# Kernel optimization log

Measured on AMD Instinct MI355X. Metric: run time of the kernel, lower is better.

## Reference

```python
import jax, jax.numpy as jnp
import numpy as np

N_NODES = 100000
N_EDGES = 1600000
HIDDEN = 64
LEAKY_SLOPE = 0.01  # torch F.leaky_relu default


def setup_inputs() -> dict:
    key = jax.random.key(0)
    k1, k2, k3, k4 = jax.random.split(key, 4)
    x = jax.random.normal(k1, (N_NODES, HIDDEN), dtype=jnp.float32)
    edge_index = jax.random.randint(k2, (2, N_EDGES), 0, N_NODES, dtype=jnp.int64)
    # Linear(hidden, 1, bias=False) weights, squeezed to [hidden]
    w_i = jax.random.normal(k3, (HIDDEN,), dtype=jnp.float32) * 0.1
    w_j = jax.random.normal(k4, (HIDDEN,), dtype=jnp.float32) * 0.1
    return {"x": x, "edge_index": edge_index, "w_i": w_i, "w_j": w_j}


def reference(x, edge_index, w_i, w_j):
    n = x.shape[0]
    ej, ei = edge_index[0], edge_index[1]  # (edge_index_j, edge_index_i)
    # per-node attention scores, then per-edge gather
    s_i = x @ w_i  # [N]
    s_j = x @ w_j  # [N]
    e = jax.nn.leaky_relu(s_i[ei] + s_j[ej], LEAKY_SLOPE)  # [E]
    # segment softmax over edges grouped by destination node ei
    emax = jax.ops.segment_max(e, ei, num_segments=n)  # [N]
    ex = jnp.exp(e - emax[ei])  # [E]
    denom = jax.ops.segment_sum(ex, ei, num_segments=n)  # [N]
    alpha = ex / denom[ei]  # [E]
    # spmm: out[i] = sum_{edges e: dst=i} alpha_e * x[src_e]
    out = jax.ops.segment_sum(alpha[:, None] * x[ej], ei, num_segments=n)  # [N, H]
    return jax.nn.relu(out)
```

## Files before the change

### kernel.cpp

```cpp
#include <hip/hip_runtime.h>
#include <stdint.h>

#define N_NODES 100000
#define N_EDGES 1600000
#define HIDDEN  64
#define SLOPE   0.01f
#define NBUCK   782
#define CAPB    2816
#define PCHUNK  16384
#define NPART   98
#define NSB     391
#define NCAP    48
#define NSTRIDE 50


__device__ __forceinline__ unsigned short f2bf(float f) {
    uint32_t u = __float_as_uint(f);
    uint32_t r = u + 0x7FFFu + ((u >> 16) & 1u);
    return (unsigned short)(r >> 16);
}

__global__ void __launch_bounds__(1024) k_build(const float* __restrict__ x,
                                                const float* __restrict__ w_i,
                                                const float* __restrict__ w_j,
                                                const int* __restrict__ srcs,
                                                const int* __restrict__ dsts,
                                                float* __restrict__ s_i,
                                                float* __restrict__ s_j,
                                                unsigned short* __restrict__ xb,
                                                int* __restrict__ ctrl,
                                                uint32_t* __restrict__ pairs) {
    __shared__ int lcnt[NBUCK], lloc[NBUCK], lbase[NBUCK];
    __shared__ int scan[1024];
    __shared__ uint32_t srec[PCHUNK];
    int tid = threadIdx.x;
    if (blockIdx.x < NPART) {
        if (blockIdx.x == 0) {
            if (tid < NBUCK) atomicExch(&ctrl[tid], 0);
            __syncthreads();
            if (tid == 0) { __threadfence(); atomicExch(&ctrl[NBUCK], 1); }
        }
        if (tid < NBUCK) lcnt[tid] = 0;
        __syncthreads();
        int e0 = blockIdx.x * PCHUNK;
        int e1 = min(e0 + PCHUNK, N_EDGES);
        for (int e = e0 + tid; e < e1; e += 1024)
            atomicAdd(&lcnt[dsts[e] >> 7], 1);
        __syncthreads();
        int v = (tid < NBUCK) ? lcnt[tid] : 0;
        scan[tid] = v;
        __syncthreads();
        for (int off = 1; off < 1024; off <<= 1) {
            int t = (tid >= off) ? scan[tid - off] : 0;
            __syncthreads();
            scan[tid] += t;
            __syncthreads();
        }
        if (tid < NBUCK) lloc[tid] = scan[tid] - v;
        if (tid == 0)
            while (atomicAdd(&ctrl[NBUCK], 0) != 1) {}
        __syncthreads();
        if (tid < NBUCK) {
            lbase[tid] = v ? atomicAdd(&ctrl[tid], v) : 0;
            lcnt[tid] = 0;
        }
        __syncthreads();
        for (int e = e0 + tid; e < e1; e += 1024) {
            int src = srcs[e];
            int dst = dsts[e];
            int b = dst >> 7;
            int r = atomicAdd(&lcnt[b], 1);
            srec[lloc[b] + r] = ((uint32_t)(dst & 127) << 24) | (uint32_t)src;
        }
        __syncthreads();
        int wv = tid >> 6, ln = tid & 63;
        for (int b = wv; b < NBUCK; b += 16) {
            int c = lcnt[b];
            int lo = lloc[b], go = lbase[b];
            for (int j = ln; j < c; j += 64) {
                int pos = go + j;
                if (pos < CAPB)
                    pairs[(size_t)b * CAPB + pos] = srec[lo + j];
            }
        }
        return;
    }
    int u0 = blockIdx.x - NPART;
    int g16 = tid >> 4;
    int ql = tid & 15;
    float4 wi4 = ((const float4*)w_i)[ql];
    float4 wj4 = ((const float4*)w_j)[ql];
#pragma unroll
    for (int i = 0; i < 4; ++i) {
        int node = u0 * 256 + i * 64 + g16;
        if (node >= N_NODES) break;
        float4 v = ((const float4*)x)[node * 16 + ql];
        float a = v.x * wi4.x + v.y * wi4.y + v.z * wi4.z + v.w * wi4.w;
        float b = v.x * wj4.x + v.y * wj4.y + v.z * wj4.z + v.w * wj4.w;
#pragma unroll
        for (int off = 1; off < 16; off <<= 1) {
            a += __shfl_xor(a, off, 64);
            b += __shfl_xor(b, off, 64);
        }
        if (ql == 0) { s_i[node] = a; s_j[node] = b; }
        ushort4 o;
        o.x = f2bf(v.x); o.y = f2bf(v.y); o.z = f2bf(v.z); o.w = f2bf(v.w);
        ((ushort4*)xb)[node * 16 + ql] = o;
    }
}

__device__ __forceinline__ float bflo(uint32_t d) { return __uint_as_float(d << 16); }
__device__ __forceinline__ float bfhi(uint32_t d) { return __uint_as_float(d & 0xFFFF0000u); }

__global__ void __launch_bounds__(1024, 8) k_bucket_agg(const uint4* __restrict__ xw4,
                                                        const uint32_t* __restrict__ pairs,
                                                        const int* __restrict__ ctrl,
                                                        const float* __restrict__ s_i,
                                                        const float* __restrict__ s_j,
                                                        float* __restrict__ out) {
    __shared__ uint64_t spairs[128 * NSTRIDE];
    __shared__ int lcur[128];
    __shared__ float s_si[128];
    int tid = threadIdx.x;
    int cb = blockIdx.x;
    int node0 = cb * 128;
    const uint32_t* reg = pairs + (size_t)cb * CAPB;
    int rcnt = min(ctrl[cb], CAPB);
    for (int i = tid; i < 128 * NSTRIDE; i += 1024) spairs[i] = 0ull;
    if (tid < 128) {
        lcur[tid] = 0;
        int node = node0 + tid;
        s_si[tid] = (node < N_NODES) ? s_i[node] : 0.f;
    }
    __syncthreads();
    {
        int e0 = tid, e1 = tid + 1024;
        bool a0 = e0 < rcnt, a1 = e1 < rcnt;
        uint32_t p0 = a0 ? reg[e0] : 0u;
        uint32_t p1 = a1 ? reg[e1] : 0u;
        float sj0 = a0 ? s_j[p0 & 0xFFFFFFu] : 0.f;
        float sj1 = a1 ? s_j[p1 & 0xFFFFFFu] : 0.f;
        if (a0) {
            int n = (int)(p0 >> 24);
            float sc = s_si[n] + sj0;
            sc = (sc > 0.f) ? sc : SLOPE * sc;
            float w = __expf(sc);
            int slot = atomicAdd(&lcur[n], 1);
            if (slot < NCAP)
                spairs[n * NSTRIDE + slot] =
                    ((uint64_t)__float_as_uint(w) << 32) | (p0 & 0xFFFFFFu);
        }
        if (a1) {
            int n = (int)(p1 >> 24);
            float sc = s_si[n] + sj1;
            sc = (sc > 0.f) ? sc : SLOPE * sc;
            float w = __expf(sc);
            int slot = atomicAdd(&lcur[n], 1);
            if (slot < NCAP)
                spairs[n * NSTRIDE + slot] =
                    ((uint64_t)__float_as_uint(w) << 32) | (p1 & 0xFFFFFFu);
        }
        for (int e = tid + 2048; e < rcnt; e += 1024) {
            uint32_t p = reg[e];
            int n = (int)(p >> 24);
            float sc = s_si[n] + s_j[p & 0xFFFFFFu];
            sc = (sc > 0.f) ? sc : SLOPE * sc;
            float w = __expf(sc);
            int slot = atomicAdd(&lcur[n], 1);
            if (slot < NCAP)
                spairs[n * NSTRIDE + slot] =
                    ((uint64_t)__float_as_uint(w) << 32) | (p & 0xFFFFFFu);
        }
    }
    __syncthreads();
    int wave = tid >> 6, lane = tid & 63;
    int quarter = (lane >> 4) & 3;
    int half8 = (lane >> 3) & 1;
    int l8 = lane & 7;
    for (int hl = 0; hl < 2; ++hl) {
        int k = wave * 4 + quarter + 64 * hl;
        int node = node0 + k;
        int creal = lcur[k];
        int cq = min(creal, NCAP);
        int mx = cq;
        mx = max(mx, __shfl_xor(mx, 16, 64));
        mx = max(mx, __shfl_xor(mx, 32, 64));
        const uint64_t* pp = spairs + k * NSTRIDE;
        float acc[8] = {0.f, 0.f, 0.f, 0.f, 0.f, 0.f, 0.f, 0.f};
        float den = 0.f;
        for (int j = 0; j < mx; j += 8) {
            uint64_t rec[4];
            uint4 d[4];
#pragma unroll
            for (int t = 0; t < 4; ++t)
                rec[t] = pp[j + 2 * t + half8];
#pragma unroll
            for (int t = 0; t < 4; ++t)
                d[t] = xw4[((uint32_t)rec[t] & 0xFFFFFFu) * 8 + l8];
#pragma unroll
            for (int t = 0; t < 4; ++t) {
                float w = __uint_as_float((uint32_t)(rec[t] >> 32));
                den += w;
                acc[0] = fmaf(w, bflo(d[t].x), acc[0]);
                acc[1] = fmaf(w, bfhi(d[t].x), acc[1]);
                acc[2] = fmaf(w, bflo(d[t].y), acc[2]);
                acc[3] = fmaf(w, bfhi(d[t].y), acc[3]);
                acc[4] = fmaf(w, bflo(d[t].z), acc[4]);
                acc[5] = fmaf(w, bfhi(d[t].z), acc[5]);
                acc[6] = fmaf(w, bflo(d[t].w), acc[6]);
                acc[7] = fmaf(w, bfhi(d[t].w), acc[7]);
            }
        }
        if (creal > NCAP) {
#pragma unroll
            for (int i = 0; i < 8; ++i) acc[i] = 0.f;
            den = 0.f;
            for (int e = 0; e < rcnt; ++e) {
                uint32_t p = reg[e];
                if ((int)(p >> 24) == k) {
                    uint32_t src = p & 0xFFFFFFu;
                    float sc = s_si[k] + s_j[src];
                    sc = (sc > 0.f) ? sc : SLOPE * sc;
                    float w = (half8 == 0) ? __expf(sc) : 0.f;
                    uint4 dd = xw4[src * 8 + l8];
                    den += w;
                    acc[0] = fmaf(w, bflo(dd.x), acc[0]);
                    acc[1] = fmaf(w, bfhi(dd.x), acc[1]);
                    acc[2] = fmaf(w, bflo(dd.y), acc[2]);
                    acc[3] = fmaf(w, bfhi(dd.y), acc[3]);
                    acc[4] = fmaf(w, bflo(dd.z), acc[4]);
                    acc[5] = fmaf(w, bfhi(dd.z), acc[5]);
                    acc[6] = fmaf(w, bflo(dd.w), acc[6]);
                    acc[7] = fmaf(w, bfhi(dd.w), acc[7]);
                }
            }
        }
#pragma unroll
        for (int i = 0; i < 8; ++i) acc[i] += __shfl_xor(acc[i], 8, 64);
        den += __shfl_xor(den, 8, 64);
        if (half8 == 0 && node < N_NODES) {
            float4 r0 = make_float4(0.f, 0.f, 0.f, 0.f);
            float4 r1 = r0;
            if (creal > 0) {
                float inv = 1.f / den;
                r0.x = fmaxf(acc[0] * inv, 0.f);
                r0.y = fmaxf(acc[1] * inv, 0.f);
                r0.z = fmaxf(acc[2] * inv, 0.f);
                r0.w = fmaxf(acc[3] * inv, 0.f);
                r1.x = fmaxf(acc[4] * inv, 0.f);
                r1.y = fmaxf(acc[5] * inv, 0.f);
                r1.z = fmaxf(acc[6] * inv, 0.f);
                r1.w = fmaxf(acc[7] * inv, 0.f);
            }
            float4* op = (float4*)(out + (size_t)node * HIDDEN + l8 * 8);
            op[0] = r0;
            op[1] = r1;
        }
    }
}

extern "C" void kernel_launch(void* const* d_in, const int* in_sizes, int n_in,
                              void* d_out, int out_size, void* d_ws, size_t ws_size,
                              hipStream_t stream) {
    const float* x   = (const float*)d_in[0];
    const int*   ei  = (const int*)d_in[1];
    const float* w_i = (const float*)d_in[2];
    const float* w_j = (const float*)d_in[3];
    float* out = (float*)d_out;

    char* p = (char*)d_ws;
    float*          s_i   = (float*)p;          p += (size_t)N_NODES * 4;
    float*          s_j   = (float*)p;          p += (size_t)N_NODES * 4;
    unsigned short* xb    = (unsigned short*)p; p += (size_t)N_NODES * HIDDEN * 2;
    int*            ctrl  = (int*)p;            p += 4096;
    uint32_t*       pairs = (uint32_t*)p;

    const int* srcs = ei;
    const int* dsts = ei + N_EDGES;

    k_build     <<<NPART + NSB, 1024, 0, stream>>>(x, w_i, w_j, srcs, dsts,
                                                   s_i, s_j, xb, ctrl, pairs);
    k_bucket_agg<<<NBUCK, 1024, 0, stream>>>((const uint4*)xb, pairs, ctrl,
                                             s_i, s_j, out);
}
```

Before: 143.2 us.

## Fuse build and aggregation into one cooperative kernel with grid sync

Merges the partition/score kernel and the bucket aggregation kernel into a single cooperative launch. A grid-wide sync separates the phases, and the two phases share shared memory through a union. It also prefetches the next edge records from LDS inside the aggregation loop. The aim is to remove the second kernel launch and its inter-kernel gap. The cost is a 489-block grid that must be co-resident, with a fallback to two launches if the cooperative launch fails. The larger shared-memory footprint may also lower occupancy in the aggregation phase.

```diff
diff --git a/kernel.cpp b/kernel.cpp
--- a/kernel.cpp
+++ b/kernel.cpp
@@ -1,5 +1,8 @@
 #include <hip/hip_runtime.h>
+#include <hip/hip_cooperative_groups.h>
 #include <stdint.h>
+
+namespace cg = cooperative_groups;
 
 #define N_NODES 100000
 #define N_EDGES 1600000
@@ -10,6 +13,7 @@
 #define PCHUNK  16384
 #define NPART   98
 #define NSB     391
+#define NGRID   (NPART + NSB)
 #define NCAP    48
 #define NSTRIDE 50
 
@@ -20,72 +24,85 @@
     return (unsigned short)(r >> 16);
 }
 
-__global__ void __launch_bounds__(1024) k_build(const float* __restrict__ x,
-                                                const float* __restrict__ w_i,
-                                                const float* __restrict__ w_j,
-                                                const int* __restrict__ srcs,
-                                                const int* __restrict__ dsts,
-                                                float* __restrict__ s_i,
-                                                float* __restrict__ s_j,
-                                                unsigned short* __restrict__ xb,
-                                                int* __restrict__ ctrl,
-                                                uint32_t* __restrict__ pairs) {
-    __shared__ int lcnt[NBUCK], lloc[NBUCK], lbase[NBUCK];
-    __shared__ int scan[1024];
-    __shared__ uint32_t srec[PCHUNK];
-    int tid = threadIdx.x;
-    if (blockIdx.x < NPART) {
-        if (blockIdx.x == 0) {
-            if (tid < NBUCK) atomicExch(&ctrl[tid], 0);
-            __syncthreads();
-            if (tid == 0) { __threadfence(); atomicExch(&ctrl[NBUCK], 1); }
-        }
-        if (tid < NBUCK) lcnt[tid] = 0;
+__device__ __forceinline__ float bflo(uint32_t d) { return __uint_as_float(d << 16); }
+__device__ __forceinline__ float bfhi(uint32_t d) { return __uint_as_float(d & 0xFFFF0000u); }
+
+struct SmemA {
+    int lcnt[NBUCK];
+    int lloc[NBUCK];
+    int lbase[NBUCK];
+    int scan[1024];
+    uint32_t srec[PCHUNK];
+};
+struct SmemB {
+    uint64_t spairs[128 * NSTRIDE];
+    int lcur[128];
+    float s_si[128];
+};
+union SmemU { SmemA a; SmemB b; };
+
+__device__ __forceinline__ void do_partition(SmemA& sa, int bid, int tid,
+                                             const int* __restrict__ srcs,
+                                             const int* __restrict__ dsts,
+                                             int* __restrict__ ctrl,
+                                             uint32_t* __restrict__ pairs) {
+    if (bid == 0) {
+        if (tid < NBUCK) atomicExch(&ctrl[tid], 0);
         __syncthreads();
-        int e0 = blockIdx.x * PCHUNK;
-        int e1 = min(e0 + PCHUNK, N_EDGES);
-        for (int e = e0 + tid; e < e1; e += 1024)
-            atomicAdd(&lcnt[dsts[e] >> 7], 1);
+        if (tid == 0) { __threadfence(); atomicExch(&ctrl[NBUCK], 1); }
+    }
+    if (tid < NBUCK) sa.lcnt[tid] = 0;
+    __syncthreads();
+    int e0 = bid * PCHUNK;
+    int e1 = min(e0 + PCHUNK, N_EDGES);
+    for (int e = e0 + tid; e < e1; e += 1024)
+        atomicAdd(&sa.lcnt[dsts[e] >> 7], 1);
+    __syncthreads();
+    int v = (tid < NBUCK) ? sa.lcnt[tid] : 0;
+    sa.scan[tid] = v;
+    __syncthreads();
+    for (int off = 1; off < 1024; off <<= 1) {
+        int t = (tid >= off) ? sa.scan[tid - off] : 0;
         __syncthreads();
-        int v = (tid < NBUCK) ? lcnt[tid] : 0;
-        scan[tid] = v;
+        sa.scan[tid] += t;
         __syncthreads();
-        for (int off = 1; off < 1024; off <<= 1) {
-            int t = (tid >= off) ? scan[tid - off] : 0;
-            __syncthreads();
-            scan[tid] += t;
-            __syncthreads();
-        }
-        if (tid < NBUCK) lloc[tid] = scan[tid] - v;
-        if (tid == 0)
-            while (atomicAdd(&ctrl[NBUCK], 0) != 1) {}
-        __syncthreads();
-        if (tid < NBUCK) {
-            lbase[tid] = v ? atomicAdd(&ctrl[tid], v) : 0;
-            lcnt[tid] = 0;
-        }
-        __syncthreads();
-        for (int e = e0 + tid; e < e1; e += 1024) {
-            int src = srcs[e];
-            int dst = dsts[e];
-            int b = dst >> 7;
-            int r = atomicAdd(&lcnt[b], 1);
-            srec[lloc[b] + r] = ((uint32_t)(dst & 127) << 24) | (uint32_t)src;
-        }
-        __syncthreads();
-        int wv = tid >> 6, ln = tid & 63;
-        for (int b = wv; b < NBUCK; b += 16) {
-            int c = lcnt[b];
-            int lo = lloc[b], go = lbase[b];
-            for (int j = ln; j < c; j += 64) {
-                int pos = go + j;
-                if (pos < CAPB)
-                    pairs[(size_t)b * CAPB + pos] = srec[lo + j];
-            }
-        }
-        return;
-    }
-    int u0 = blockIdx.x - NPART;
+    }
+    if (tid < NBUCK) sa.lloc[tid] = sa.scan[tid] - v;
+    if (tid == 0)
+        while (atomicAdd(&ctrl[NBUCK], 0) != 1) {}
+    __syncthreads();
+    if (tid < NBUCK) {
+        sa.lbase[tid] = v ? atomicAdd(&ctrl[tid], v) : 0;
+        sa.lcnt[tid] = 0;
+    }
+    __syncthreads();
+    for (int e = e0 + tid; e < e1; e += 1024) {
+        int src = srcs[e];
+        int dst = dsts[e];
+        int b = dst >> 7;
+        int r = atomicAdd(&sa.lcnt[b], 1);
+        sa.srec[sa.lloc[b] + r] = ((uint32_t)(dst & 127) << 24) | (uint32_t)src;
+    }
+    __syncthreads();
+    int wv = tid >> 6, ln = tid & 63;
+    for (int b = wv; b < NBUCK; b += 16) {
+        int c = sa.lcnt[b];
+        int lo = sa.lloc[b], go = sa.lbase[b];
+        for (int j = ln; j < c; j += 64) {
+            int pos = go + j;
+            if (pos < CAPB)
+                pairs[(size_t)b * CAPB + pos] = sa.srec[lo + j];
+        }
+    }
+}
+
+__device__ __forceinline__ void do_scores(int u0, int tid,
+                                          const float* __restrict__ x,
+                                          const float* __restrict__ w_i,
+                                          const float* __restrict__ w_j,
+                                          float* __restrict__ s_i,
+                                          float* __restrict__ s_j,
+                                          unsigned short* __restrict__ xb) {
     int g16 = tid >> 4;
     int ql = tid & 15;
     float4 wi4 = ((const float4*)w_i)[ql];
@@ -109,28 +126,22 @@
     }
 }
 
-__device__ __forceinline__ float bflo(uint32_t d) { return __uint_as_float(d << 16); }
-__device__ __forceinline__ float bfhi(uint32_t d) { return __uint_as_float(d & 0xFFFF0000u); }
-
-__global__ void __launch_bounds__(1024, 8) k_bucket_agg(const uint4* __restrict__ xw4,
-                                                        const uint32_t* __restrict__ pairs,
-                                                        const int* __restrict__ ctrl,
-                                                        const float* __restrict__ s_i,
-                                                        const float* __restrict__ s_j,
-                                                        float* __restrict__ out) {
-    __shared__ uint64_t spairs[128 * NSTRIDE];
-    __shared__ int lcur[128];
-    __shared__ float s_si[128];
-    int tid = threadIdx.x;
-    int cb = blockIdx.x;
+__device__ __forceinline__ void agg_bucket(SmemB& sb, int cb, int tid,
+                                           const uint4* __restrict__ xw4,
+                                           const uint32_t* __restrict__ pairs,
+                                           const int* __restrict__ ctrl,
+                                           const float* __restrict__ s_i,
+                                           const float* __restrict__ s_j,
+                                           float* __restrict__ out) {
     int node0 = cb * 128;
     const uint32_t* reg = pairs + (size_t)cb * CAPB;
     int rcnt = min(ctrl[cb], CAPB);
-    for (int i = tid; i < 128 * NSTRIDE; i += 1024) spairs[i] = 0ull;
+    __syncthreads();
+    for (int i = tid; i < 128 * NSTRIDE; i += 1024) sb.spairs[i] = 0ull;
     if (tid < 128) {
-        lcur[tid] = 0;
+        sb.lcur[tid] = 0;
         int node = node0 + tid;
-        s_si[tid] = (node < N_NODES) ? s_i[node] : 0.f;
+        sb.s_si[tid] = (node < N_NODES) ? s_i[node] : 0.f;
     }
     __syncthreads();
     {
@@ -142,33 +153,33 @@
         float sj1 = a1 ? s_j[p1 & 0xFFFFFFu] : 0.f;
         if (a0) {
             int n = (int)(p0 >> 24);
-            float sc = s_si[n] + sj0;
+            float sc = sb.s_si[n] + sj0;
             sc = (sc > 0.f) ? sc : SLOPE * sc;
             float w = __expf(sc);
-            int slot = atomicAdd(&lcur[n], 1);
+            int slot = atomicAdd(&sb.lcur[n], 1);
             if (slot < NCAP)
-                spairs[n * NSTRIDE + slot] =
+                sb.spairs[n * NSTRIDE + slot] =
                     ((uint64_t)__float_as_uint(w) << 32) | (p0 & 0xFFFFFFu);
         }
         if (a1) {
             int n = (int)(p1 >> 24);
-            float sc = s_si[n] + sj1;
+            float sc = sb.s_si[n] + sj1;
             sc = (sc > 0.f) ? sc : SLOPE * sc;
             float w = __expf(sc);
-            int slot = atomicAdd(&lcur[n], 1);
+            int slot = atomicAdd(&sb.lcur[n], 1);
             if (slot < NCAP)
-                spairs[n * NSTRIDE + slot] =
+                sb.spairs[n * NSTRIDE + slot] =
                     ((uint64_t)__float_as_uint(w) << 32) | (p1 & 0xFFFFFFu);
         }
         for (int e = tid + 2048; e < rcnt; e += 1024) {
             uint32_t p = reg[e];
             int n = (int)(p >> 24);
-            float sc = s_si[n] + s_j[p & 0xFFFFFFu];
+            float sc = sb.s_si[n] + s_j[p & 0xFFFFFFu];
             sc = (sc > 0.f) ? sc : SLOPE * sc;
             float w = __expf(sc);
-            int slot = atomicAdd(&lcur[n], 1);
+            int slot = atomicAdd(&sb.lcur[n], 1);
             if (slot < NCAP)
-                spairs[n * NSTRIDE + slot] =
+                sb.spairs[n * NSTRIDE + slot] =
                     ((uint64_t)__float_as_uint(w) << 32) | (p & 0xFFFFFFu);
         }
     }
@@ -180,23 +191,27 @@
     for (int hl = 0; hl < 2; ++hl) {
         int k = wave * 4 + quarter + 64 * hl;
         int node = node0 + k;
-        int creal = lcur[k];
+        int creal = sb.lcur[k];
         int cq = min(creal, NCAP);
         int mx = cq;
         mx = max(mx, __shfl_xor(mx, 16, 64));
         mx = max(mx, __shfl_xor(mx, 32, 64));
-        const uint64_t* pp = spairs + k * NSTRIDE;
+        const uint64_t* pp = sb.spairs + k * NSTRIDE;
         float acc[8] = {0.f, 0.f, 0.f, 0.f, 0.f, 0.f, 0.f, 0.f};
         float den = 0.f;
+        uint64_t rec[4];
+#pragma unroll
+        for (int t = 0; t < 4; ++t) rec[t] = pp[2 * t + half8];
         for (int j = 0; j < mx; j += 8) {
-            uint64_t rec[4];
             uint4 d[4];
-#pragma unroll
-            for (int t = 0; t < 4; ++t)
-                rec[t] = pp[j + 2 * t + half8];
 #pragma unroll
             for (int t = 0; t < 4; ++t)
                 d[t] = xw4[((uint32_t)rec[t] & 0xFFFFFFu) * 8 + l8];
+            int jn = j + 8;
+            const uint64_t* pn = pp + ((jn < mx) ? jn : 0);
+            uint64_t nrec[4];
+#pragma unroll
+            for (int t = 0; t < 4; ++t) nrec[t] = pn[2 * t + half8];
 #pragma unroll
             for (int t = 0; t < 4; ++t) {
                 float w = __uint_as_float((uint32_t)(rec[t] >> 32));
@@ -210,6 +225,8 @@
                 acc[6] = fmaf(w, bflo(d[t].w), acc[6]);
                 acc[7] = fmaf(w, bfhi(d[t].w), acc[7]);
             }
+#pragma unroll
+            for (int t = 0; t < 4; ++t) rec[t] = nrec[t];
         }
         if (creal > NCAP) {
 #pragma unroll
@@ -219,7 +236,7 @@
                 uint32_t p = reg[e];
                 if ((int)(p >> 24) == k) {
                     uint32_t src = p & 0xFFFFFFu;
-                    float sc = s_si[k] + s_j[src];
+                    float sc = sb.s_si[k] + s_j[src];
                     sc = (sc > 0.f) ? sc : SLOPE * sc;
                     float w = (half8 == 0) ? __expf(sc) : 0.f;
                     uint4 dd = xw4[src * 8 + l8];
@@ -259,6 +276,57 @@
     }
 }
 
+__global__ void __launch_bounds__(1024, 8) k_fused(const float* __restrict__ x,
+                                                   const float* __restrict__ w_i,
+                                                   const float* __restrict__ w_j,
+                                                   const int* __restrict__ srcs,
+                                                   const int* __restrict__ dsts,
+                                                   float* __restrict__ s_i,
+                                                   float* __restrict__ s_j,
+                                                   unsigned short* __restrict__ xb,
+                                                   int* __restrict__ ctrl,
+                                                   uint32_t* __restrict__ pairs,
+                                                   float* __restrict__ out) {
+    __shared__ SmemU sm;
+    int tid = threadIdx.x;
+    int bid = blockIdx.x;
+    if (bid < NPART)
+        do_partition(sm.a, bid, tid, srcs, dsts, ctrl, pairs);
+    else
+        do_scores(bid - NPART, tid, x, w_i, w_j, s_i, s_j, xb);
+    cg::this_grid().sync();
+    for (int cb = bid; cb < NBUCK; cb += NGRID)
+        agg_bucket(sm.b, cb, tid, (const uint4*)xb, pairs, ctrl, s_i, s_j, out);
+}
+
+__global__ void __launch_bounds__(1024) k_build(const float* __restrict__ x,
+                                                const float* __restrict__ w_i,
+                                                const float* __restrict__ w_j,
+                                                const int* __restrict__ srcs,
+                                                const int* __restrict__ dsts,
+                                                float* __restrict__ s_i,
+                                                float* __restrict__ s_j,
+                                                unsigned short* __restrict__ xb,
+                                                int* __restrict__ ctrl,
+                                                uint32_t* __restrict__ pairs) {
+    __shared__ SmemA sa;
+    int tid = threadIdx.x;
+    if (blockIdx.x < NPART)
+        do_partition(sa, blockIdx.x, tid, srcs, dsts, ctrl, pairs);
+    else
+        do_scores(blockIdx.x - NPART, tid, x, w_i, w_j, s_i, s_j, xb);
+}
+
+__global__ void __launch_bounds__(1024, 8) k_bucket_agg(const uint4* __restrict__ xw4,
+                                                        const uint32_t* __restrict__ pairs,
+                                                        const int* __restrict__ ctrl,
+                                                        const float* __restrict__ s_i,
+                                                        const float* __restrict__ s_j,
+                                                        float* __restrict__ out) {
+    __shared__ SmemB sb;
+    agg_bucket(sb, blockIdx.x, threadIdx.x, xw4, pairs, ctrl, s_i, s_j, out);
+}
+
 extern "C" void kernel_launch(void* const* d_in, const int* in_sizes, int n_in,
                               void* d_out, int out_size, void* d_ws, size_t ws_size,
                               hipStream_t stream) {
@@ -278,8 +346,15 @@
     const int* srcs = ei;
     const int* dsts = ei + N_EDGES;
 
-    k_build     <<<NPART + NSB, 1024, 0, stream>>>(x, w_i, w_j, srcs, dsts,
-                                                   s_i, s_j, xb, ctrl, pairs);
-    k_bucket_agg<<<NBUCK, 1024, 0, stream>>>((const uint4*)xb, pairs, ctrl,
-                                             s_i, s_j, out);
-}
+    void* kargs[] = { (void*)&x, (void*)&w_i, (void*)&w_j, (void*)&srcs, (void*)&dsts,
+                      (void*)&s_i, (void*)&s_j, (void*)&xb, (void*)&ctrl, (void*)&pairs,
+                      (void*)&out };
+    hipError_t err = hipLaunchCooperativeKernel((const void*)k_fused, dim3(NGRID),
+                                                dim3(1024), kargs, 0, stream);
+    if (err != hipSuccess) {
+        k_build     <<<NPART + NSB, 1024, 0, stream>>>(x, w_i, w_j, srcs, dsts,
+                                                       s_i, s_j, xb, ctrl, pairs);
+        k_bucket_agg<<<NBUCK, 1024, 0, stream>>>((const uint4*)xb, pairs, ctrl,
+                                                 s_i, s_j, out);
+    }
+}
```

After: 228.4 us. 1.6x slower.

## Prefetch next edge batch in aggregation, halve partition chunks, memset counters

Applied to the files above, without the earlier changes.

The aggregation loop is software-pipelined so that the pair records and bf16 feature rows for the next 8 edges load while the FMAs run on the current batch. The edge partition chunk is halved and the number of partition blocks doubled, giving more parallelism in the bucketing phase at the cost of more global atomics on bucket counters. The in-kernel counter reset by block 0, and the spin-wait every block did on it, are replaced by a hipMemsetAsync before launch. That adds a small extra stream operation but removes a serialisation point between blocks. The prefetch also raises register pressure in the aggregation kernel.

```diff
diff --git a/kernel.cpp b/kernel.cpp
--- a/kernel.cpp
+++ b/kernel.cpp
@@ -7,8 +7,8 @@
 #define SLOPE   0.01f
 #define NBUCK   782
 #define CAPB    2816
-#define PCHUNK  16384
-#define NPART   98
+#define PCHUNK  8192
+#define NPART   196
 #define NSB     391
 #define NCAP    48
 #define NSTRIDE 50
@@ -19,6 +19,9 @@
     uint32_t r = u + 0x7FFFu + ((u >> 16) & 1u);
     return (unsigned short)(r >> 16);
 }
+
+__device__ __forceinline__ float bflo(uint32_t d) { return __uint_as_float(d << 16); }
+__device__ __forceinline__ float bfhi(uint32_t d) { return __uint_as_float(d & 0xFFFF0000u); }
 
 __global__ void __launch_bounds__(1024) k_build(const float* __restrict__ x,
                                                 const float* __restrict__ w_i,
@@ -35,11 +38,6 @@
     __shared__ uint32_t srec[PCHUNK];
     int tid = threadIdx.x;
     if (blockIdx.x < NPART) {
-        if (blockIdx.x == 0) {
-            if (tid < NBUCK) atomicExch(&ctrl[tid], 0);
-            __syncthreads();
-            if (tid == 0) { __threadfence(); atomicExch(&ctrl[NBUCK], 1); }
-        }
         if (tid < NBUCK) lcnt[tid] = 0;
         __syncthreads();
         int e0 = blockIdx.x * PCHUNK;
@@ -57,8 +55,6 @@
             __syncthreads();
         }
         if (tid < NBUCK) lloc[tid] = scan[tid] - v;
-        if (tid == 0)
-            while (atomicAdd(&ctrl[NBUCK], 0) != 1) {}
         __syncthreads();
         if (tid < NBUCK) {
             lbase[tid] = v ? atomicAdd(&ctrl[tid], v) : 0;
@@ -108,9 +104,6 @@
         ((ushort4*)xb)[node * 16 + ql] = o;
     }
 }
-
-__device__ __forceinline__ float bflo(uint32_t d) { return __uint_as_float(d << 16); }
-__device__ __forceinline__ float bfhi(uint32_t d) { return __uint_as_float(d & 0xFFFF0000u); }
 
 __global__ void __launch_bounds__(1024, 8) k_bucket_agg(const uint4* __restrict__ xw4,
                                                         const uint32_t* __restrict__ pairs,
@@ -188,28 +181,48 @@
         const uint64_t* pp = spairs + k * NSTRIDE;
         float acc[8] = {0.f, 0.f, 0.f, 0.f, 0.f, 0.f, 0.f, 0.f};
         float den = 0.f;
+        float wc[4];
+        uint4 dc[4];
+        {
+            uint64_t r0[4];
+#pragma unroll
+            for (int t = 0; t < 4; ++t) r0[t] = pp[2 * t + half8];
+#pragma unroll
+            for (int t = 0; t < 4; ++t)
+                dc[t] = xw4[((uint32_t)r0[t] & 0xFFFFFFu) * 8 + l8];
+#pragma unroll
+            for (int t = 0; t < 4; ++t)
+                wc[t] = __uint_as_float((uint32_t)(r0[t] >> 32));
+        }
         for (int j = 0; j < mx; j += 8) {
-            uint64_t rec[4];
-            uint4 d[4];
-#pragma unroll
-            for (int t = 0; t < 4; ++t)
-                rec[t] = pp[j + 2 * t + half8];
-#pragma unroll
-            for (int t = 0; t < 4; ++t)
-                d[t] = xw4[((uint32_t)rec[t] & 0xFFFFFFu) * 8 + l8];
+            int jn = j + 8;
+            const uint64_t* pn = pp + ((jn < mx) ? jn : 0);
+            uint64_t rn[4];
+            uint4 dn[4];
+            float wn[4];
+#pragma unroll
+            for (int t = 0; t < 4; ++t) rn[t] = pn[2 * t + half8];
+#pragma unroll
+            for (int t = 0; t < 4; ++t)
+                dn[t] = xw4[((uint32_t)rn[t] & 0xFFFFFFu) * 8 + l8];
+#pragma unroll
+            for (int t = 0; t < 4; ++t)
+                wn[t] = __uint_as_float((uint32_t)(rn[t] >> 32));
 #pragma unroll
             for (int t = 0; t < 4; ++t) {
-                float w = __uint_as_float((uint32_t)(rec[t] >> 32));
+                float w = wc[t];
                 den += w;
-                acc[0] = fmaf(w, bflo(d[t].x), acc[0]);
-                acc[1] = fmaf(w, bfhi(d[t].x), acc[1]);
-                acc[2] = fmaf(w, bflo(d[t].y), acc[2]);
-                acc[3] = fmaf(w, bfhi(d[t].y), acc[3]);
-                acc[4] = fmaf(w, bflo(d[t].z), acc[4]);
-                acc[5] = fmaf(w, bfhi(d[t].z), acc[5]);
-                acc[6] = fmaf(w, bflo(d[t].w), acc[6]);
-                acc[7] = fmaf(w, bfhi(d[t].w), acc[7]);
-            }
+                acc[0] = fmaf(w, bflo(dc[t].x), acc[0]);
+                acc[1] = fmaf(w, bfhi(dc[t].x), acc[1]);
+                acc[2] = fmaf(w, bflo(dc[t].y), acc[2]);
+                acc[3] = fmaf(w, bfhi(dc[t].y), acc[3]);
+                acc[4] = fmaf(w, bflo(dc[t].z), acc[4]);
+                acc[5] = fmaf(w, bfhi(dc[t].z), acc[5]);
+                acc[6] = fmaf(w, bflo(dc[t].w), acc[6]);
+                acc[7] = fmaf(w, bfhi(dc[t].w), acc[7]);
+            }
+#pragma unroll
+            for (int t = 0; t < 4; ++t) { dc[t] = dn[t]; wc[t] = wn[t]; }
         }
         if (creal > NCAP) {
 #pragma unroll
@@ -278,6 +291,7 @@
     const int* srcs = ei;
     const int* dsts = ei + N_EDGES;
 
+    hipMemsetAsync(ctrl, 0, (NBUCK + 1) * sizeof(int), stream);
     k_build     <<<NPART + NSB, 1024, 0, stream>>>(x, w_i, w_j, srcs, dsts,
                                                    s_i, s_j, xb, ctrl, pairs);
     k_bucket_agg<<<NBUCK, 1024, 0, stream>>>((const uint4*)xb, pairs, ctrl,
```

After: 145.5 us. No clear change (+1.6%).

## Use 16-lane per-node gather with two nodes per quarter-wave; memset control counters

Applied to the files above, without the earlier changes.

The aggregation loop now assigns 16 lanes per node, each loading 8 bytes (4 bf16 features). Each quarter-wave handles two nodes at once, interleaving their gathers so more independent loads are in flight, and the half-lane split with its cross-lane shuffle reduction is removed. The in-kernel zeroing of bucket counters and the spin-wait on a ready flag are replaced by a hipMemsetAsync before the build kernel. This trades an extra stream operation for dropping the intra-kernel cross-block synchronization, and uses narrower per-lane loads.

```diff
diff --git a/kernel.cpp b/kernel.cpp
--- a/kernel.cpp
+++ b/kernel.cpp
@@ -19,6 +19,9 @@
     uint32_t r = u + 0x7FFFu + ((u >> 16) & 1u);
     return (unsigned short)(r >> 16);
 }
+
+__device__ __forceinline__ float bflo(uint32_t d) { return __uint_as_float(d << 16); }
+__device__ __forceinline__ float bfhi(uint32_t d) { return __uint_as_float(d & 0xFFFF0000u); }
 
 __global__ void __launch_bounds__(1024) k_build(const float* __restrict__ x,
                                                 const float* __restrict__ w_i,
@@ -35,11 +38,6 @@
     __shared__ uint32_t srec[PCHUNK];
     int tid = threadIdx.x;
     if (blockIdx.x < NPART) {
-        if (blockIdx.x == 0) {
-            if (tid < NBUCK) atomicExch(&ctrl[tid], 0);
-            __syncthreads();
-            if (tid == 0) { __threadfence(); atomicExch(&ctrl[NBUCK], 1); }
-        }
         if (tid < NBUCK) lcnt[tid] = 0;
         __syncthreads();
         int e0 = blockIdx.x * PCHUNK;
@@ -57,8 +55,6 @@
             __syncthreads();
         }
         if (tid < NBUCK) lloc[tid] = scan[tid] - v;
-        if (tid == 0)
-            while (atomicAdd(&ctrl[NBUCK], 0) != 1) {}
         __syncthreads();
         if (tid < NBUCK) {
             lbase[tid] = v ? atomicAdd(&ctrl[tid], v) : 0;
@@ -109,10 +105,7 @@
     }
 }
 
-__device__ __forceinline__ float bflo(uint32_t d) { return __uint_as_float(d << 16); }
-__device__ __forceinline__ float bfhi(uint32_t d) { return __uint_as_float(d & 0xFFFF0000u); }
-
-__global__ void __launch_bounds__(1024, 8) k_bucket_agg(const uint4* __restrict__ xw4,
+__global__ void __launch_bounds__(1024, 8) k_bucket_agg(const uint2* __restrict__ xw2,
                                                         const uint32_t* __restrict__ pairs,
                                                         const int* __restrict__ ctrl,
                                                         const float* __restrict__ s_i,
@@ -175,87 +168,112 @@
     __syncthreads();
     int wave = tid >> 6, lane = tid & 63;
     int quarter = (lane >> 4) & 3;
-    int half8 = (lane >> 3) & 1;
-    int l8 = lane & 7;
-    for (int hl = 0; hl < 2; ++hl) {
-        int k = wave * 4 + quarter + 64 * hl;
-        int node = node0 + k;
-        int creal = lcur[k];
-        int cq = min(creal, NCAP);
-        int mx = cq;
-        mx = max(mx, __shfl_xor(mx, 16, 64));
-        mx = max(mx, __shfl_xor(mx, 32, 64));
-        const uint64_t* pp = spairs + k * NSTRIDE;
-        float acc[8] = {0.f, 0.f, 0.f, 0.f, 0.f, 0.f, 0.f, 0.f};
-        float den = 0.f;
-        for (int j = 0; j < mx; j += 8) {
-            uint64_t rec[4];
-            uint4 d[4];
-#pragma unroll
-            for (int t = 0; t < 4; ++t)
-                rec[t] = pp[j + 2 * t + half8];
-#pragma unroll
-            for (int t = 0; t < 4; ++t)
-                d[t] = xw4[((uint32_t)rec[t] & 0xFFFFFFu) * 8 + l8];
-#pragma unroll
-            for (int t = 0; t < 4; ++t) {
-                float w = __uint_as_float((uint32_t)(rec[t] >> 32));
-                den += w;
-                acc[0] = fmaf(w, bflo(d[t].x), acc[0]);
-                acc[1] = fmaf(w, bfhi(d[t].x), acc[1]);
-                acc[2] = fmaf(w, bflo(d[t].y), acc[2]);
-                acc[3] = fmaf(w, bfhi(d[t].y), acc[3]);
-                acc[4] = fmaf(w, bflo(d[t].z), acc[4]);
-                acc[5] = fmaf(w, bfhi(d[t].z), acc[5]);
-                acc[6] = fmaf(w, bflo(d[t].w), acc[6]);
-                acc[7] = fmaf(w, bfhi(d[t].w), acc[7]);
+    int l16 = lane & 15;
+    int kA = wave * 8 + quarter;
+    int kB = kA + 4;
+    int nodeA = node0 + kA, nodeB = node0 + kB;
+    int cA = lcur[kA], cB = lcur[kB];
+    int cqA = min(cA, NCAP), cqB = min(cB, NCAP);
+    int mx = max(cqA, cqB);
+    mx = max(mx, __shfl_xor(mx, 16, 64));
+    mx = max(mx, __shfl_xor(mx, 32, 64));
+    const uint64_t* ppA = spairs + kA * NSTRIDE;
+    const uint64_t* ppB = spairs + kB * NSTRIDE;
+    float accA[4] = {0.f, 0.f, 0.f, 0.f};
+    float accB[4] = {0.f, 0.f, 0.f, 0.f};
+    float denA = 0.f, denB = 0.f;
+    for (int j = 0; j < mx; j += 4) {
+        uint64_t rA[4], rB[4];
+#pragma unroll
+        for (int t = 0; t < 4; ++t) { rA[t] = ppA[j + t]; rB[t] = ppB[j + t]; }
+        uint2 dA[4], dB[4];
+#pragma unroll
+        for (int t = 0; t < 4; ++t)
+            dA[t] = xw2[((uint32_t)rA[t] & 0xFFFFFFu) * 16 + l16];
+#pragma unroll
+        for (int t = 0; t < 4; ++t)
+            dB[t] = xw2[((uint32_t)rB[t] & 0xFFFFFFu) * 16 + l16];
+        __builtin_amdgcn_sched_barrier(0);
+#pragma unroll
+        for (int t = 0; t < 4; ++t) {
+            float w = __uint_as_float((uint32_t)(rA[t] >> 32));
+            denA += w;
+            accA[0] = fmaf(w, bflo(dA[t].x), accA[0]);
+            accA[1] = fmaf(w, bfhi(dA[t].x), accA[1]);
+            accA[2] = fmaf(w, bflo(dA[t].y), accA[2]);
+            accA[3] = fmaf(w, bfhi(dA[t].y), accA[3]);
+        }
+#pragma unroll
+        for (int t = 0; t < 4; ++t) {
+            float w = __uint_as_float((uint32_t)(rB[t] >> 32));
+            denB += w;
+            accB[0] = fmaf(w, bflo(dB[t].x), accB[0]);
+            accB[1] = fmaf(w, bfhi(dB[t].x), accB[1]);
+            accB[2] = fmaf(w, bflo(dB[t].y), accB[2]);
+            accB[3] = fmaf(w, bfhi(dB[t].y), accB[3]);
+        }
+    }
+    if (cA > NCAP) {
+        denA = 0.f;
+#pragma unroll
+        for (int i = 0; i < 4; ++i) accA[i] = 0.f;
+        for (int e = 0; e < rcnt; ++e) {
+            uint32_t p = reg[e];
+            if ((int)(p >> 24) == kA) {
+                uint32_t src = p & 0xFFFFFFu;
+                float sc = s_si[kA] + s_j[src];
+                sc = (sc > 0.f) ? sc : SLOPE * sc;
+                float w = __expf(sc);
+                uint2 d = xw2[src * 16 + l16];
+                denA += w;
+                accA[0] = fmaf(w, bflo(d.x), accA[0]);
+                accA[1] = fmaf(w, bfhi(d.x), accA[1]);
+                accA[2] = fmaf(w, bflo(d.y), accA[2]);
+                accA[3] = fmaf(w, bfhi(d.y), accA[3]);
             }
         }
-        if (creal > NCAP) {
-#pragma unroll
-            for (int i = 0; i < 8; ++i) acc[i] = 0.f;
-            den = 0.f;
-            for (int e = 0; e < rcnt; ++e) {
-                uint32_t p = reg[e];
-                if ((int)(p >> 24) == k) {
-                    uint32_t src = p & 0xFFFFFFu;
-                    float sc = s_si[k] + s_j[src];
-                    sc = (sc > 0.f) ? sc : SLOPE * sc;
-                    float w = (half8 == 0) ? __expf(sc) : 0.f;
-                    uint4 dd = xw4[src * 8 + l8];
-                    den += w;
-                    acc[0] = fmaf(w, bflo(dd.x), acc[0]);
-                    acc[1] = fmaf(w, bfhi(dd.x), acc[1]);
-                    acc[2] = fmaf(w, bflo(dd.y), acc[2]);
-                    acc[3] = fmaf(w, bfhi(dd.y), acc[3]);
-                    acc[4] = fmaf(w, bflo(dd.z), acc[4]);
-                    acc[5] = fmaf(w, bfhi(dd.z), acc[5]);
-                    acc[6] = fmaf(w, bflo(dd.w), acc[6]);
-                    acc[7] = fmaf(w, bfhi(dd.w), acc[7]);
-                }
+    }
+    if (cB > NCAP) {
+        denB = 0.f;
+#pragma unroll
+        for (int i = 0; i < 4; ++i) accB[i] = 0.f;
+        for (int e = 0; e < rcnt; ++e) {
+            uint32_t p = reg[e];
+            if ((int)(p >> 24) == kB) {
+                uint32_t src = p & 0xFFFFFFu;
+                float sc = s_si[kB] + s_j[src];
+                sc = (sc > 0.f) ? sc : SLOPE * sc;
+                float w = __expf(sc);
+                uint2 d = xw2[src * 16 + l16];
+                denB += w;
+                accB[0] = fmaf(w, bflo(d.x), accB[0]);
+                accB[1] = fmaf(w, bfhi(d.x), accB[1]);
+                accB[2] = fmaf(w, bflo(d.y), accB[2]);
+                accB[3] = fmaf(w, bfhi(d.y), accB[3]);
             }
         }
-#pragma unroll
-        for (int i = 0; i < 8; ++i) acc[i] += __shfl_xor(acc[i], 8, 64);
-        den += __shfl_xor(den, 8, 64);
-        if (half8 == 0 && node < N_NODES) {
-            float4 r0 = make_float4(0.f, 0.f, 0.f, 0.f);
-            float4 r1 = r0;
-            if (creal > 0) {
-                float inv = 1.f / den;
-                r0.x = fmaxf(acc[0] * inv, 0.f);
-                r0.y = fmaxf(acc[1] * inv, 0.f);
-                r0.z = fmaxf(acc[2] * inv, 0.f);
-                r0.w = fmaxf(acc[3] * inv, 0.f);
-                r1.x = fmaxf(acc[4] * inv, 0.f);
-                r1.y = fmaxf(acc[5] * inv, 0.f);
-                r1.z = fmaxf(acc[6] * inv, 0.f);
-                r1.w = fmaxf(acc[7] * inv, 0.f);
-            }
-            float4* op = (float4*)(out + (size_t)node * HIDDEN + l8 * 8);
-            op[0] = r0;
-            op[1] = r1;
-        }
+    }
+    if (nodeA < N_NODES) {
+        float4 r = make_float4(0.f, 0.f, 0.f, 0.f);
+        if (cA > 0) {
+            float inv = 1.f / denA;
+            r.x = fmaxf(accA[0] * inv, 0.f);
+            r.y = fmaxf(accA[1] * inv, 0.f);
+            r.z = fmaxf(accA[2] * inv, 0.f);
+            r.w = fmaxf(accA[3] * inv, 0.f);
+        }
+        ((float4*)(out + (size_t)nodeA * HIDDEN))[l16] = r;
+    }
+    if (nodeB < N_NODES) {
+        float4 r = make_float4(0.f, 0.f, 0.f, 0.f);
+        if (cB > 0) {
+            float inv = 1.f / denB;
+            r.x = fmaxf(accB[0] * inv, 0.f);
+            r.y = fmaxf(accB[1] * inv, 0.f);
+            r.z = fmaxf(accB[2] * inv, 0.f);
+            r.w = fmaxf(accB[3] * inv, 0.f);
+        }
+        ((float4*)(out + (size_t)nodeB * HIDDEN))[l16] = r;
     }
 }
 
@@ -278,8 +296,9 @@
     const int* srcs = ei;
     const int* dsts = ei + N_EDGES;
 
+    hipMemsetAsync(ctrl, 0, (NBUCK + 1) * sizeof(int), stream);
     k_build     <<<NPART + NSB, 1024, 0, stream>>>(x, w_i, w_j, srcs, dsts,
                                                    s_i, s_j, xb, ctrl, pairs);
-    k_bucket_agg<<<NBUCK, 1024, 0, stream>>>((const uint4*)xb, pairs, ctrl,
+    k_bucket_agg<<<NBUCK, 1024, 0, stream>>>((const uint2*)xb, pairs, ctrl,
                                              s_i, s_j, out);
 }
```

Measured after the change: 149.3 us. 1.04x slower.
